# Kernel optimization log

Measured on AMD Instinct MI355X. Metric: run time of the kernel, lower is better.

## Reference

```python
import jax, jax.numpy as jnp
import numpy as np

B, T, F = 64, 96, 32          # batch, window_size, num_features
H_ENC, H_DEC = 128, 128       # encoder / decoder hidden sizes


def _lstm_cell(x, h, c, k, r, b):
    # Keras LSTMCell math: gates ordered i, f, g(candidate), o
    z = x @ k + h @ r + b
    i, f, g, o = jnp.split(z, 4, axis=-1)
    i = jax.nn.sigmoid(i)
    f = jax.nn.sigmoid(f)
    g = jnp.tanh(g)
    o = jax.nn.sigmoid(o)
    c_new = f * c + i * g
    h_new = o * jnp.tanh(c_new)
    return h_new, c_new


def setup_inputs() -> dict:
    key = jax.random.key(0)
    ks = jax.random.split(key, 20)
    s = 0.05
    d = {
        "inputs": jax.random.normal(ks[0], (B, T, F), jnp.float32),
        # encoder LSTMCell (input dim = F)
        "enc_k": jax.random.normal(ks[1], (F, 4 * H_ENC), jnp.float32) * s,
        "enc_r": jax.random.normal(ks[2], (H_ENC, 4 * H_ENC), jnp.float32) * s,
        "enc_b": jnp.zeros((4 * H_ENC,), jnp.float32),
        # encoder attention MLP: in = 2*H_ENC + T -> H_ENC -> 1
        "ae_w1": jax.random.normal(ks[3], (2 * H_ENC + T, H_ENC), jnp.float32) * s,
        "ae_b1": jnp.zeros((H_ENC,), jnp.float32),
        "ae_w2": jax.random.normal(ks[4], (H_ENC, 1), jnp.float32) * s,
        "ae_b2": jnp.zeros((1,), jnp.float32),
        # decoder LSTMCell (input dim = H_DEC, the fc output)
        "dec_k": jax.random.normal(ks[5], (H_DEC, 4 * H_DEC), jnp.float32) * s,
        "dec_r": jax.random.normal(ks[6], (H_DEC, 4 * H_DEC), jnp.float32) * s,
        "dec_b": jnp.zeros((4 * H_DEC,), jnp.float32),
        # decoder attention MLP: in = 2*H_DEC + H_ENC -> H_ENC -> 1
        "ad_w1": jax.random.normal(ks[7], (2 * H_DEC + H_ENC, H_ENC), jnp.float32) * s,
        "ad_b1": jnp.zeros((H_ENC,), jnp.float32),
        "ad_w2": jax.random.normal(ks[8], (H_ENC, 1), jnp.float32) * s,
        "ad_b2": jnp.zeros((1,), jnp.float32),
        # fc: (context H_ENC + y_prev 1) -> H_DEC
        "fc_w": jax.random.normal(ks[9], (H_ENC + 1, H_DEC), jnp.float32) * s,
        "fc_b": jnp.zeros((H_DEC,), jnp.float32),
        # fc_final: (d_n H_DEC + context H_ENC) -> F
        "ff_w": jax.random.normal(ks[10], (H_DEC + H_ENC, F), jnp.float32) * s,
        "ff_b": jnp.zeros((F,), jnp.float32),
    }
    return d


def reference(inputs, enc_k, enc_r, enc_b, ae_w1, ae_b1, ae_w2, ae_b2,
              dec_k, dec_r, dec_b, ad_w1, ad_b1, ad_w2, ad_b2,
              fc_w, fc_b, ff_w, ff_b):
    b, t, f = inputs.shape
    h_enc = enc_r.shape[0]
    h_dec = dec_r.shape[0]
    x_perm = jnp.transpose(inputs, (0, 2, 1))  # [B, F, T] (constant over time)

    # ---------------- encoder: input-attention LSTM over time ----------------
    def enc_step(carry, x_t):
        h, s = carry  # each [B, H_enc]
        hb = jnp.broadcast_to(h[:, None, :], (b, f, h_enc))
        sb = jnp.broadcast_to(s[:, None, :], (b, f, h_enc))
        cat = jnp.concatenate([hb, sb, x_perm], axis=2)       # [B, F, 2H+T]
        e = jnp.tanh(cat @ ae_w1 + ae_b1) @ ae_w2 + ae_b2     # [B, F, 1]
        alpha = jax.nn.softmax(e[..., 0], axis=1)             # [B, F]
        x_tilde = alpha * x_t                                 # [B, F]
        h, s = _lstm_cell(x_tilde, h, s, enc_k, enc_r, enc_b)
        return (h, s), h

    init = (jnp.zeros((b, h_enc), inputs.dtype), jnp.zeros((b, h_enc), inputs.dtype))
    _, h_all = jax.lax.scan(enc_step, init, jnp.transpose(inputs, (1, 0, 2)))
    x_encoded = jnp.transpose(h_all, (1, 0, 2))               # [B, T, H_enc]

    # ---------------- decoder: temporal-attention LSTM over time -------------
    y_prev = inputs[:, :, -1]                                 # [B, T]

    def dec_step(carry, y_t):
        d, c, _ = carry
        db = jnp.broadcast_to(d[:, None, :], (b, t, h_dec))
        cb = jnp.broadcast_to(c[:, None, :], (b, t, h_dec))
        cat = jnp.concatenate([db, cb, x_encoded], axis=2)    # [B, T, 2Hd+He]
        e = jnp.tanh(cat @ ad_w1 + ad_b1) @ ad_w2 + ad_b2     # [B, T, 1]
        beta = jax.nn.softmax(e[..., 0], axis=1)              # [B, T]
        ctx = jnp.einsum("bt,bth->bh", beta, x_encoded)       # [B, H_enc]
        y_tilde = jnp.concatenate([ctx, y_t[:, None]], axis=1) @ fc_w + fc_b
        d, c = _lstm_cell(y_tilde, d, c, dec_k, dec_r, dec_b)
        return (d, c, ctx), None

    init_d = (jnp.zeros((b, h_dec), inputs.dtype),
              jnp.zeros((b, h_dec), inputs.dtype),
              jnp.zeros((b, h_enc), inputs.dtype))
    (d_n, _, ctx), _ = jax.lax.scan(dec_step, init_d, jnp.transpose(y_prev, (1, 0)))

    y_pred = jnp.concatenate([d_n, ctx], axis=1) @ ff_w + ff_b  # [B, F]
    return y_pred[:, None, :]                                   # [B, 1, F]
```

## Files before the change

### kernel.cpp

```cpp
#include <hip/hip_runtime.h>

#define TT 96
#define FF 32
#define HH 128
#define G4 512
#define LOG2E 1.4426950408889634f

typedef _Float16 h2 __attribute__((ext_vector_type(2)));

__device__ __forceinline__ float fexp2(float x){ return __builtin_amdgcn_exp2f(x); }
__device__ __forceinline__ float frcp(float x){ return __builtin_amdgcn_rcpf(x); }
__device__ __forceinline__ float fsigmoid(float x){ return frcp(1.0f + fexp2(-LOG2E*x)); }
__device__ __forceinline__ float ftanh(float x){
    float u = fexp2(2.0f*LOG2E*x);
    return 1.0f - 2.0f*frcp(1.0f + u);
}
__device__ __forceinline__ h2 pk(float a, float b){
    h2 r; r.x = (_Float16)a; r.y = (_Float16)b; return r;
}
__device__ __forceinline__ unsigned pku(float a, float b){
    return __builtin_bit_cast(unsigned, pk(a, b));
}
__device__ __forceinline__ h2 u2h(unsigned v){ return __builtin_bit_cast(h2, v); }
__device__ __forceinline__ float fdot2(h2 a, h2 b, float c){
#if __has_builtin(__builtin_amdgcn_fdot2)
    return __builtin_amdgcn_fdot2(a, b, c, false);
#else
    return c + (float)a.x*(float)b.x + (float)a.y*(float)b.y;
#endif
}

__global__ __launch_bounds__(256) void k_prep(const float* __restrict__ fc_w,
                                              const float* __restrict__ fc_b,
                                              const float* __restrict__ dec_k,
                                              const float* __restrict__ dec_b,
                                              h2* __restrict__ Gp,
                                              float* __restrict__ gy,
                                              float* __restrict__ gb){
    int blk = blockIdx.x, tid = threadIdx.x;
    int u0 = tid, u1 = tid + 256;
    if (blk < 16){
        float a0[8], a1[8];
        #pragma unroll
        for (int r = 0; r < 8; ++r){ a0[r] = 0.f; a1[r] = 0.f; }
        for (int m = 0; m < 128; ++m){
            float d0 = dec_k[m*G4 + u0], d1 = dec_k[m*G4 + u1];
            #pragma unroll
            for (int r = 0; r < 8; ++r){
                float w = fc_w[(blk*8 + r)*HH + m];
                a0[r] += w * d0; a1[r] += w * d1;
            }
        }
        #pragma unroll
        for (int c = 0; c < 4; ++c){
            Gp[(blk*G4 + u0)*4 + c] = pk(a0[2*c], a0[2*c+1]);
            Gp[(blk*G4 + u1)*4 + c] = pk(a1[2*c], a1[2*c+1]);
        }
    } else if (blk == 16){
        float a0 = 0.f, a1 = 0.f;
        for (int m = 0; m < 128; ++m){
            float w = fc_w[128*HH + m];
            a0 += w * dec_k[m*G4 + u0]; a1 += w * dec_k[m*G4 + u1];
        }
        gy[u0] = a0; gy[u1] = a1;
    } else {
        float a0 = 0.f, a1 = 0.f;
        for (int m = 0; m < 128; ++m){
            float w = fc_b[m];
            a0 += w * dec_k[m*G4 + u0]; a1 += w * dec_k[m*G4 + u1];
        }
        gb[u0] = a0 + dec_b[u0]; gb[u1] = a1 + dec_b[u1];
    }
}

__global__ __launch_bounds__(1024)
__attribute__((amdgpu_waves_per_eu(4, 4)))
void k_enc(const float* __restrict__ inputs,
           const float* __restrict__ enc_k,
           const float* __restrict__ enc_r,
           const float* __restrict__ enc_b,
           const float* __restrict__ ae_w1,
           const float* __restrict__ ae_b1,
           const float* __restrict__ ae_w2,
           const float* __restrict__ ad_w1,
           float* __restrict__ ws_xenc,
           float* __restrict__ ws_xept){
    extern __shared__ float lds[];
    uint4* KLH4 = (uint4*)lds;
    float* XPJT = lds + 8192;
    float* XIN  = lds + 12416;
    float* HST  = lds + 15488;
    float* PP   = lds + 15744;
    float* PPZ  = lds + 16768;
    float* PE   = lds + 17792;
    float* W2E  = lds + 17920;
    float* AB1E = lds + 18048;
    h2*    HSP  = (h2*)(lds + 18176);
    h2*    XTP  = (h2*)(lds + 18240);
    uint4* WAE4 = (uint4*)(lds + 18256);
    _Float16* XEF = (_Float16*)(lds + 34640);

    const int b = blockIdx.x, tid = threadIdx.x;
    const int u = tid & 511, hf = tid >> 9;
    const int j7 = tid & 127, g8 = tid >> 7;
    const float* xin_g = inputs + b*TT*FF;

    for (int i = tid; i < TT*FF; i += 1024) XIN[i] = xin_g[i];
    for (int i = tid; i < 2048; i += 1024){
        int f8 = i >> 9, uu = i & 511;
        uint4 q;
        q.x = pku(enc_k[(f8*8+0)*G4+uu], enc_k[(f8*8+1)*G4+uu]);
        q.y = pku(enc_k[(f8*8+2)*G4+uu], enc_k[(f8*8+3)*G4+uu]);
        q.z = pku(enc_k[(f8*8+4)*G4+uu], enc_k[(f8*8+5)*G4+uu]);
        q.w = pku(enc_k[(f8*8+6)*G4+uu], enc_k[(f8*8+7)*G4+uu]);
        KLH4[i] = q;
    }
    for (int i = tid; i < 4096; i += 1024){
        int j = i & 127, i4g = i >> 7;
        int kbase = (i4g >> 2)*32 + (i4g & 3)*8;
        uint4 wv;
        wv.x = pku(ae_w1[(kbase+0)*HH + j], ae_w1[(kbase+1)*HH + j]);
        wv.y = pku(ae_w1[(kbase+2)*HH + j], ae_w1[(kbase+3)*HH + j]);
        wv.z = pku(ae_w1[(kbase+4)*HH + j], ae_w1[(kbase+5)*HH + j]);
        wv.w = pku(ae_w1[(kbase+6)*HH + j], ae_w1[(kbase+7)*HH + j]);
        WAE4[i] = wv;
    }
    if (tid < 128){ W2E[tid] = ae_w2[tid]; AB1E[tid] = ae_b1[tid]; HSP[tid] = pk(0.f, 0.f); }
    if (tid < 256) HST[tid] = 0.f;

    h2 rp_e[32];
    #pragma unroll
    for (int i = 0; i < 32; ++i)
        rp_e[i] = pk(enc_r[(hf*64 + 2*i)*G4 + u], enc_r[(hf*64 + 2*i+1)*G4 + u]);
    const float eb = (hf == 0) ? enc_b[u] : 0.f;
    __syncthreads();

    {
        int j = tid & 127, fh = tid >> 7;
        float a0=0.f, a1=0.f, a2=0.f, a3=0.f;
        for (int t = 0; t < TT; ++t){
            float w = ae_w1[(256 + t)*HH + j];
            const float* xr = &XIN[t*FF + fh*4];
            a0 += xr[0]*w; a1 += xr[1]*w; a2 += xr[2]*w; a3 += xr[3]*w;
        }
        XPJT[j*33 + fh*4 + 0] = a0;
        XPJT[j*33 + fh*4 + 1] = a1;
        XPJT[j*33 + fh*4 + 2] = a2;
        XPJT[j*33 + fh*4 + 3] = a3;
    }
    __syncthreads();

    const uint4* HSP4 = (const uint4*)HSP;
    const uint4* XTP4 = (const uint4*)XTP;

    for (int t = 0; t < TT; ++t){
        {
            float a0 = 0.f, a1 = 0.f;
            #pragma unroll
            for (int i4 = 0; i4 < 4; ++i4){
                uint4 q  = HSP4[g8*4 + i4];
                uint4 wv = WAE4[(g8*4 + i4)*128 + j7];
                a0 = fdot2(u2h(q.x), u2h(wv.x), a0);
                a1 = fdot2(u2h(q.y), u2h(wv.y), a1);
                a0 = fdot2(u2h(q.z), u2h(wv.z), a0);
                a1 = fdot2(u2h(q.w), u2h(wv.w), a1);
            }
            PP[tid] = a0 + a1;
        }
        float z = eb;
        {
            float z2 = 0.f;
            #pragma unroll
            for (int i4 = 0; i4 < 8; ++i4){
                uint4 q = HSP4[hf*8 + i4];
                z  = fdot2(u2h(q.x), rp_e[i4*4+0], z);
                z2 = fdot2(u2h(q.y), rp_e[i4*4+1], z2);
                z  = fdot2(u2h(q.z), rp_e[i4*4+2], z);
                z2 = fdot2(u2h(q.w), rp_e[i4*4+3], z2);
            }
            z += z2;
        }
        __syncthreads();
        if (tid < 128){
            float s = AB1E[tid];
            #pragma unroll
            for (int g = 0; g < 8; ++g) s += PP[tid + 128*g];
            PE[tid] = s;
        }
        __syncthreads();
        {
            int f = tid & 31, jg = tid >> 5;
            float acc = 0.f;
            #pragma unroll
            for (int i = 0; i < 4; ++i){
                int j = jg*4 + i;
                acc += ftanh(PE[j] + XPJT[j*33 + f]) * W2E[j];
            }
            PP[tid] = acc;
        }
        __syncthreads();
        if (tid < 32){
            float e = 0.f;
            #pragma unroll
            for (int g = 0; g < 32; ++g) e += PP[g*32 + tid];
            float p = fexp2(e * LOG2E);
            float ss = p;
            #pragma unroll
            for (int d = 16; d; d >>= 1) ss += __shfl_xor(ss, d, 32);
            float xt = p * frcp(ss) * XIN[t*FF + tid];
            float xt2 = __shfl_xor(xt, 1);
            if (!(tid & 1)) XTP[tid >> 1] = pk(xt, xt2);
        }
        __syncthreads();
        {
            float z2 = 0.f;
            #pragma unroll
            for (int c = 0; c < 2; ++c){
                int f8 = hf*2 + c;
                uint4 kq = KLH4[f8*512 + u];
                uint4 xq = XTP4[f8];
                z  = fdot2(u2h(kq.x), u2h(xq.x), z);
                z2 = fdot2(u2h(kq.y), u2h(xq.y), z2);
                z  = fdot2(u2h(kq.z), u2h(xq.z), z);
                z2 = fdot2(u2h(kq.w), u2h(xq.w), z2);
            }
            PPZ[hf*512 + u] = z + z2;
        }
        __syncthreads();
        if (tid < 128){
            int j = tid;
            float zi = PPZ[j]       + PPZ[512 + j];
            float zf = PPZ[128 + j] + PPZ[640 + j];
            float zg = PPZ[256 + j] + PPZ[768 + j];
            float zo = PPZ[384 + j] + PPZ[896 + j];
            float iv = fsigmoid(zi);
            float fv = fsigmoid(zf);
            float gv = ftanh(zg);
            float ov = fsigmoid(zo);
            float cn = fv * HST[128 + j] + iv * gv;
            float hn = ov * ftanh(cn);
            HST[128 + j] = cn;
            HST[j] = hn;
            ws_xenc[(b*TT + t)*HH + j] = hn;
            XEF[t*HH + j] = (_Float16)hn;
            float hn2 = __shfl_xor(hn, 1);
            float cn2 = __shfl_xor(cn, 1);
            if (!(j & 1)){
                HSP[j >> 1]        = pk(hn, hn2);
                HSP[64 + (j >> 1)] = pk(cn, cn2);
            }
        }
        __syncthreads();
    }

    {
        int j = tid & 127, th = tid >> 7;
        float acc[12];
        #pragma unroll
        for (int i = 0; i < 12; ++i) acc[i] = 0.f;
        for (int k = 0; k < 128; ++k){
            float w = ad_w1[(256 + k)*HH + j];
            #pragma unroll
            for (int i = 0; i < 12; ++i)
                acc[i] += (float)XEF[(th*12 + i)*HH + k] * w;
        }
        #pragma unroll
        for (int i = 0; i < 12; ++i)
            ws_xept[(b*HH + j)*TT + th*12 + i] = acc[i];
    }
}

__global__ __launch_bounds__(1024)
__attribute__((amdgpu_waves_per_eu(4, 4)))
void k_dec(const float* __restrict__ inputs,
           const float* __restrict__ dec_r,
           const float* __restrict__ ad_w1,
           const float* __restrict__ ad_b1,
           const float* __restrict__ ad_w2,
           const float* __restrict__ ff_w,
           const float* __restrict__ ff_b,
           const h2* __restrict__ Gp,
           const float* __restrict__ gy,
           const float* __restrict__ gb,
           const float* __restrict__ ws_xenc,
           const float* __restrict__ ws_xept,
           float* __restrict__ out){
    extern __shared__ float lds[];
    uint4* XE4 = (uint4*)lds;
    uint4* WDC4= (uint4*)(lds + 6144);
    float* PP  = lds + 22528;
    float* PPZ = lds + 23552;
    float* PPA = lds + 24576;
    float* APJ = lds + 25600;
    float* DST = lds + 25728;
    float* CTX = lds + 25984;
    float* W2L = lds + 26112;
    float* YV  = lds + 26240;
    float* SCAL= lds + 26336;
    h2*    DCP = (h2*)(lds + 26344);
    h2*    CXP = (h2*)(lds + 26408);
    h2*    BEP = (h2*)(lds + 26440);

    const int b = blockIdx.x, tid = threadIdx.x;
    const int u = tid & 511, hf = tid >> 9;
    const int j = tid & 127, og = tid >> 7;

    {
        const float* xe_g = ws_xenc + b*TT*HH;
        for (int i = tid; i < 12*HH; i += 1024){
            int t8 = i >> 7, k = i & 127;
            uint4 qq;
            qq.x = pku(xe_g[(t8*8 + 0)*HH + k], xe_g[(t8*8 + 1)*HH + k]);
            qq.y = pku(xe_g[(t8*8 + 2)*HH + k], xe_g[(t8*8 + 3)*HH + k]);
            qq.z = pku(xe_g[(t8*8 + 4)*HH + k], xe_g[(t8*8 + 5)*HH + k]);
            qq.w = pku(xe_g[(t8*8 + 6)*HH + k], xe_g[(t8*8 + 7)*HH + k]);
            XE4[i] = qq;
        }
    }
    for (int i = tid; i < 4096; i += 1024){
        int jj = i & 127, i4g = i >> 7;
        int kbase = (i4g >> 2)*32 + (i4g & 3)*8;
        uint4 wv;
        wv.x = pku(ad_w1[(kbase+0)*HH + jj], ad_w1[(kbase+1)*HH + jj]);
        wv.y = pku(ad_w1[(kbase+2)*HH + jj], ad_w1[(kbase+3)*HH + jj]);
        wv.z = pku(ad_w1[(kbase+4)*HH + jj], ad_w1[(kbase+5)*HH + jj]);
        wv.w = pku(ad_w1[(kbase+6)*HH + jj], ad_w1[(kbase+7)*HH + jj]);
        WDC4[i] = wv;
    }
    if (tid < TT) YV[tid] = inputs[b*TT*FF + tid*FF + (FF-1)];
    if (tid < 128){ W2L[tid] = ad_w2[tid]; DCP[tid] = pk(0.f, 0.f); }
    if (tid < 256) DST[tid] = 0.f;

    h2 rp[32];
    #pragma unroll
    for (int i = 0; i < 32; ++i)
        rp[i] = pk(dec_r[(hf*64 + 2*i)*G4 + u], dec_r[(hf*64 + 2*i+1)*G4 + u]);

    uint4 Greg[8];
    {
        const uint4* GQ = (const uint4*)Gp;
        #pragma unroll
        for (int g = 0; g < 8; ++g) Greg[g] = GQ[(hf*8 + g)*G4 + u];
    }

    float xpr[16];
    {
        const float* xp_g = ws_xept + (b*HH + og*16)*TT + j;
        if (j < TT){
            #pragma unroll
            for (int i = 0; i < 16; ++i) xpr[i] = xp_g[i*TT];
        } else {
            #pragma unroll
            for (int i = 0; i < 16; ++i) xpr[i] = 0.f;
        }
    }

    const float gbr = gb[u], gyr = gy[u];
    const float ab1 = (tid < 128) ? ad_b1[tid] : 0.f;
    __syncthreads();

    const uint4* DCP4 = (const uint4*)DCP;
    const uint4* CXP4 = (const uint4*)CXP;
    const uint4* BEP4 = (const uint4*)BEP;

    for (int t = 0; t < TT; ++t){
        float z = (hf == 0) ? (gbr + YV[t]*gyr) : 0.f;
        {
            float z2 = 0.f;
            #pragma unroll
            for (int i4 = 0; i4 < 8; ++i4){
                uint4 q = DCP4[hf*8 + i4];
                z  = fdot2(u2h(q.x), rp[i4*4+0], z);
                z2 = fdot2(u2h(q.y), rp[i4*4+1], z2);
                z  = fdot2(u2h(q.z), rp[i4*4+2], z);
                z2 = fdot2(u2h(q.w), rp[i4*4+3], z2);
            }
            z += z2;
        }
        {
            float s0 = 0.f, s1 = 0.f;
            #pragma unroll
            for (int i = 0; i < 4; ++i){
                uint4 dq = DCP4[og*4 + i];
                uint4 wv = WDC4[(og*4 + i)*128 + j];
                s0 = fdot2(u2h(dq.x), u2h(wv.x), s0);
                s1 = fdot2(u2h(dq.y), u2h(wv.y), s1);
                s0 = fdot2(u2h(dq.z), u2h(wv.z), s0);
                s1 = fdot2(u2h(dq.w), u2h(wv.w), s1);
            }
            PPA[og*128 + j] = s0 + s1;
        }
        __syncthreads();
        if (tid < 128){
            float s = ab1;
            #pragma unroll
            for (int g = 0; g < 8; ++g) s += PPA[tid + 128*g];
            APJ[tid] = s;
        }
        __syncthreads();
        {
            float acc = 0.f;
            if (j < TT){
                #pragma unroll
                for (int q4 = 0; q4 < 4; ++q4){
                    float4 aj = *(const float4*)&APJ[og*16 + q4*4];
                    float4 wj = *(const float4*)&W2L[og*16 + q4*4];
                    acc += ftanh(aj.x + xpr[q4*4+0]) * wj.x;
                    acc += ftanh(aj.y + xpr[q4*4+1]) * wj.y;
                    acc += ftanh(aj.z + xpr[q4*4+2]) * wj.z;
                    acc += ftanh(aj.w + xpr[q4*4+3]) * wj.w;
                }
            }
            PP[tid] = acc;
        }
        __syncthreads();
        if (tid < 64){
            float ea = 0.f;
            #pragma unroll
            for (int g = 0; g < 8; ++g) ea += PP[tid + 128*g];
            float pa = fexp2(ea * LOG2E);
            float pb = 0.f;
            if (tid < 32){
                float ebv = 0.f;
                #pragma unroll
                for (int g = 0; g < 8; ++g) ebv += PP[64 + tid + 128*g];
                pb = fexp2(ebv * LOG2E);
            }
            float ss = pa + pb;
            #pragma unroll
            for (int d = 32; d; d >>= 1) ss += __shfl_xor(ss, d, 64);
            float pa2 = __shfl_xor(pa, 1);
            float pb2 = __shfl_xor(pb, 1);
            if (!(tid & 1)){
                BEP[tid >> 1] = pk(pa, pa2);
                if (tid < 32) BEP[32 + (tid >> 1)] = pk(pb, pb2);
            }
            if (tid == 0) SCAL[0] = frcp(ss);
        }
        __syncthreads();
        if (tid < 128){
            float s0 = 0.f, s1 = 0.f;
            #pragma unroll
            for (int t8 = 0; t8 < 12; t8 += 2){
                uint4 xq0 = XE4[t8*HH + tid],     bb0 = BEP4[t8];
                uint4 xq1 = XE4[(t8+1)*HH + tid], bb1 = BEP4[t8+1];
                s0 = fdot2(u2h(xq0.x), u2h(bb0.x), s0);
                s1 = fdot2(u2h(xq0.y), u2h(bb0.y), s1);
                s0 = fdot2(u2h(xq0.z), u2h(bb0.z), s0);
                s1 = fdot2(u2h(xq0.w), u2h(bb0.w), s1);
                s0 = fdot2(u2h(xq1.x), u2h(bb1.x), s0);
                s1 = fdot2(u2h(xq1.y), u2h(bb1.y), s1);
                s0 = fdot2(u2h(xq1.z), u2h(bb1.z), s0);
                s1 = fdot2(u2h(xq1.w), u2h(bb1.w), s1);
            }
            float cv = (s0 + s1) * SCAL[0];
            CTX[tid] = cv;
            float cv2 = __shfl_xor(cv, 1);
            if (!(tid & 1)) CXP[tid >> 1] = pk(cv, cv2);
        }
        __syncthreads();
        {
            float z2 = 0.f;
            #pragma unroll
            for (int gi = 0; gi < 8; ++gi){
                uint4 q  = Greg[gi];
                uint4 cc = CXP4[hf*8 + gi];
                z  = fdot2(u2h(q.x), u2h(cc.x), z);
                z2 = fdot2(u2h(q.y), u2h(cc.y), z2);
                z  = fdot2(u2h(q.z), u2h(cc.z), z);
                z2 = fdot2(u2h(q.w), u2h(cc.w), z2);
            }
            PPZ[hf*512 + u] = z + z2;
        }
        __syncthreads();
        if (tid < 128){
            int jj = tid;
            float zi = PPZ[jj]       + PPZ[512 + jj];
            float zf = PPZ[128 + jj] + PPZ[640 + jj];
            float zg = PPZ[256 + jj] + PPZ[768 + jj];
            float zo = PPZ[384 + jj] + PPZ[896 + jj];
            float iv = fsigmoid(zi);
            float fv = fsigmoid(zf);
            float gv = ftanh(zg);
            float ov = fsigmoid(zo);
            float cn = fv * DST[128 + jj] + iv * gv;
            float hn = ov * ftanh(cn);
            DST[128 + jj] = cn;
            DST[jj] = hn;
            float hn2 = __shfl_xor(hn, 1);
            float cn2 = __shfl_xor(cn, 1);
            if (!(jj & 1)){
                DCP[jj >> 1]        = pk(hn, hn2);
                DCP[64 + (jj >> 1)] = pk(cn, cn2);
            }
        }
        __syncthreads();
    }

    {
        int jp = tid & 31, sg = tid >> 5;
        float a = 0.f;
        #pragma unroll
        for (int kk = 0; kk < 8; ++kk){
            int k = sg*8 + kk;
            float val = (k < 128) ? DST[k] : CTX[k - 128];
            a += val * ff_w[k*FF + jp];
        }
        PP[sg*32 + jp] = a;
    }
    __syncthreads();
    if (tid < 32){
        float o = ff_b[tid];
        #pragma unroll
        for (int s = 0; s < 32; ++s) o += PP[s*32 + tid];
        out[b*FF + tid] = o;
    }
}

extern "C" void kernel_launch(void* const* d_in, const int* in_sizes, int n_in,
                              void* d_out, int out_size, void* d_ws, size_t ws_size,
                              hipStream_t stream) {
    const float* inputs = (const float*)d_in[0];
    const float* enc_k  = (const float*)d_in[1];
    const float* enc_r  = (const float*)d_in[2];
    const float* enc_b  = (const float*)d_in[3];
    const float* ae_w1  = (const float*)d_in[4];
    const float* ae_b1  = (const float*)d_in[5];
    const float* ae_w2  = (const float*)d_in[6];
    const float* dec_k  = (const float*)d_in[8];
    const float* dec_r  = (const float*)d_in[9];
    const float* dec_b  = (const float*)d_in[10];
    const float* ad_w1  = (const float*)d_in[11];
    const float* ad_b1  = (const float*)d_in[12];
    const float* ad_w2  = (const float*)d_in[13];
    const float* fc_w   = (const float*)d_in[15];
    const float* fc_b   = (const float*)d_in[16];
    const float* ff_w   = (const float*)d_in[17];
    const float* ff_b   = (const float*)d_in[18];

    float* ws      = (float*)d_ws;
    float* ws_xenc = ws;
    float* ws_xept = ws + 786432;
    h2*    Gp      = (h2*)(ws + 1572864);
    float* gy      = ws + 1605632;
    float* gb      = ws + 1606144;

    hipFuncSetAttribute((const void*)k_enc, hipFuncAttributeMaxDynamicSharedMemorySize, 163136);
    hipFuncSetAttribute((const void*)k_dec, hipFuncAttributeMaxDynamicSharedMemorySize, 105888);

    k_prep<<<18, 256, 0, stream>>>(fc_w, fc_b, dec_k, dec_b, Gp, gy, gb);
    k_enc<<<64, 1024, 163136, stream>>>(inputs, enc_k, enc_r, enc_b, ae_w1, ae_b1, ae_w2,
                                        ad_w1, ws_xenc, ws_xept);
    k_dec<<<64, 1024, 105888, stream>>>(inputs, dec_r, ad_w1, ad_b1, ad_w2, ff_w, ff_b,
                                        Gp, gy, gb, ws_xenc, ws_xept, (float*)d_out);
}
```

Baseline: 810.1 us.

## Remove per-step barriers by computing attention projections on fewer threads

In both the encoder and decoder recurrences, the 1024-thread split-K dot product for the attention projection, which wrote partials to LDS and reduced them after a barrier, is replaced. Now 128 threads each compute the full 256-length dot product, which removes one __syncthreads per timestep and the partial-sum buffer. In the decoder, the softmax normalisation and the context reduction are merged into one 64-lane wave, dropping a second barrier and the SCAL slot. The waves_per_eu attribute is replaced with launch_bounds(1024,1). This trades more serial work per thread for fewer block-wide synchronisations on the latency-bound recurrent path.

```diff
diff --git a/kernel.cpp b/kernel.cpp
--- a/kernel.cpp
+++ b/kernel.cpp
@@ -73,8 +73,7 @@
     }
 }
 
-__global__ __launch_bounds__(1024)
-__attribute__((amdgpu_waves_per_eu(4, 4)))
+__global__ __launch_bounds__(1024, 1)
 void k_enc(const float* __restrict__ inputs,
            const float* __restrict__ enc_k,
            const float* __restrict__ enc_r,
@@ -102,7 +101,6 @@
 
     const int b = blockIdx.x, tid = threadIdx.x;
     const int u = tid & 511, hf = tid >> 9;
-    const int j7 = tid & 127, g8 = tid >> 7;
     const float* xin_g = inputs + b*TT*FF;
 
     for (int i = tid; i < TT*FF; i += 1024) XIN[i] = xin_g[i];
@@ -154,19 +152,6 @@
     const uint4* XTP4 = (const uint4*)XTP;
 
     for (int t = 0; t < TT; ++t){
-        {
-            float a0 = 0.f, a1 = 0.f;
-            #pragma unroll
-            for (int i4 = 0; i4 < 4; ++i4){
-                uint4 q  = HSP4[g8*4 + i4];
-                uint4 wv = WAE4[(g8*4 + i4)*128 + j7];
-                a0 = fdot2(u2h(q.x), u2h(wv.x), a0);
-                a1 = fdot2(u2h(q.y), u2h(wv.y), a1);
-                a0 = fdot2(u2h(q.z), u2h(wv.z), a0);
-                a1 = fdot2(u2h(q.w), u2h(wv.w), a1);
-            }
-            PP[tid] = a0 + a1;
-        }
         float z = eb;
         {
             float z2 = 0.f;
@@ -180,12 +165,22 @@
             }
             z += z2;
         }
-        __syncthreads();
         if (tid < 128){
-            float s = AB1E[tid];
-            #pragma unroll
-            for (int g = 0; g < 8; ++g) s += PP[tid + 128*g];
-            PE[tid] = s;
+            float s0 = 0.f, s1 = 0.f;
+            #pragma unroll
+            for (int m = 0; m < 32; m += 2){
+                uint4 dq0 = HSP4[m],     wv0 = WAE4[m*128 + tid];
+                uint4 dq1 = HSP4[m + 1], wv1 = WAE4[(m + 1)*128 + tid];
+                s0 = fdot2(u2h(dq0.x), u2h(wv0.x), s0);
+                s1 = fdot2(u2h(dq0.y), u2h(wv0.y), s1);
+                s0 = fdot2(u2h(dq0.z), u2h(wv0.z), s0);
+                s1 = fdot2(u2h(dq0.w), u2h(wv0.w), s1);
+                s0 = fdot2(u2h(dq1.x), u2h(wv1.x), s0);
+                s1 = fdot2(u2h(dq1.y), u2h(wv1.y), s1);
+                s0 = fdot2(u2h(dq1.z), u2h(wv1.z), s0);
+                s1 = fdot2(u2h(dq1.w), u2h(wv1.w), s1);
+            }
+            PE[tid] = s0 + s1 + AB1E[tid];
         }
         __syncthreads();
         {
@@ -270,8 +265,7 @@
     }
 }
 
-__global__ __launch_bounds__(1024)
-__attribute__((amdgpu_waves_per_eu(4, 4)))
+__global__ __launch_bounds__(1024, 1)
 void k_dec(const float* __restrict__ inputs,
            const float* __restrict__ dec_r,
            const float* __restrict__ ad_w1,
@@ -290,16 +284,14 @@
     uint4* WDC4= (uint4*)(lds + 6144);
     float* PP  = lds + 22528;
     float* PPZ = lds + 23552;
-    float* PPA = lds + 24576;
-    float* APJ = lds + 25600;
-    float* DST = lds + 25728;
-    float* CTX = lds + 25984;
-    float* W2L = lds + 26112;
-    float* YV  = lds + 26240;
-    float* SCAL= lds + 26336;
-    h2*    DCP = (h2*)(lds + 26344);
-    h2*    CXP = (h2*)(lds + 26408);
-    h2*    BEP = (h2*)(lds + 26440);
+    float* APJ = lds + 24576;
+    float* DST = lds + 24704;
+    float* CTX = lds + 24960;
+    float* W2L = lds + 25088;
+    float* YV  = lds + 25216;
+    h2*    DCP = (h2*)(lds + 25312);
+    h2*    CXP = (h2*)(lds + 25440);
+    h2*    BEP = (h2*)(lds + 25504);
 
     const int b = blockIdx.x, tid = threadIdx.x;
     const int u = tid & 511, hf = tid >> 9;
@@ -377,25 +369,22 @@
             }
             z += z2;
         }
-        {
+        if (tid < 128){
             float s0 = 0.f, s1 = 0.f;
             #pragma unroll
-            for (int i = 0; i < 4; ++i){
-                uint4 dq = DCP4[og*4 + i];
-                uint4 wv = WDC4[(og*4 + i)*128 + j];
-                s0 = fdot2(u2h(dq.x), u2h(wv.x), s0);
-                s1 = fdot2(u2h(dq.y), u2h(wv.y), s1);
-                s0 = fdot2(u2h(dq.z), u2h(wv.z), s0);
-                s1 = fdot2(u2h(dq.w), u2h(wv.w), s1);
-            }
-            PPA[og*128 + j] = s0 + s1;
-        }
-        __syncthreads();
-        if (tid < 128){
-            float s = ab1;
-            #pragma unroll
-            for (int g = 0; g < 8; ++g) s += PPA[tid + 128*g];
-            APJ[tid] = s;
+            for (int m = 0; m < 32; m += 2){
+                uint4 dq0 = DCP4[m],     wv0 = WDC4[m*128 + tid];
+                uint4 dq1 = DCP4[m + 1], wv1 = WDC4[(m + 1)*128 + tid];
+                s0 = fdot2(u2h(dq0.x), u2h(wv0.x), s0);
+                s1 = fdot2(u2h(dq0.y), u2h(wv0.y), s1);
+                s0 = fdot2(u2h(dq0.z), u2h(wv0.z), s0);
+                s1 = fdot2(u2h(dq0.w), u2h(wv0.w), s1);
+                s0 = fdot2(u2h(dq1.x), u2h(wv1.x), s0);
+                s1 = fdot2(u2h(dq1.y), u2h(wv1.y), s1);
+                s0 = fdot2(u2h(dq1.z), u2h(wv1.z), s0);
+                s1 = fdot2(u2h(dq1.w), u2h(wv1.w), s1);
+            }
+            APJ[tid] = s0 + s1 + ab1;
         }
         __syncthreads();
         {
@@ -415,48 +404,51 @@
         }
         __syncthreads();
         if (tid < 64){
+            int l = tid;
             float ea = 0.f;
             #pragma unroll
-            for (int g = 0; g < 8; ++g) ea += PP[tid + 128*g];
+            for (int g = 0; g < 8; ++g) ea += PP[l + 128*g];
             float pa = fexp2(ea * LOG2E);
             float pb = 0.f;
-            if (tid < 32){
+            if (l < 32){
                 float ebv = 0.f;
                 #pragma unroll
-                for (int g = 0; g < 8; ++g) ebv += PP[64 + tid + 128*g];
+                for (int g = 0; g < 8; ++g) ebv += PP[64 + l + 128*g];
                 pb = fexp2(ebv * LOG2E);
             }
             float ss = pa + pb;
             #pragma unroll
             for (int d = 32; d; d >>= 1) ss += __shfl_xor(ss, d, 64);
+            float rs = frcp(ss);
             float pa2 = __shfl_xor(pa, 1);
             float pb2 = __shfl_xor(pb, 1);
-            if (!(tid & 1)){
-                BEP[tid >> 1] = pk(pa, pa2);
-                if (tid < 32) BEP[32 + (tid >> 1)] = pk(pb, pb2);
-            }
-            if (tid == 0) SCAL[0] = frcp(ss);
-        }
-        __syncthreads();
-        if (tid < 128){
-            float s0 = 0.f, s1 = 0.f;
-            #pragma unroll
-            for (int t8 = 0; t8 < 12; t8 += 2){
-                uint4 xq0 = XE4[t8*HH + tid],     bb0 = BEP4[t8];
-                uint4 xq1 = XE4[(t8+1)*HH + tid], bb1 = BEP4[t8+1];
-                s0 = fdot2(u2h(xq0.x), u2h(bb0.x), s0);
-                s1 = fdot2(u2h(xq0.y), u2h(bb0.y), s1);
-                s0 = fdot2(u2h(xq0.z), u2h(bb0.z), s0);
-                s1 = fdot2(u2h(xq0.w), u2h(bb0.w), s1);
-                s0 = fdot2(u2h(xq1.x), u2h(bb1.x), s0);
-                s1 = fdot2(u2h(xq1.y), u2h(bb1.y), s1);
-                s0 = fdot2(u2h(xq1.z), u2h(bb1.z), s0);
-                s1 = fdot2(u2h(xq1.w), u2h(bb1.w), s1);
-            }
-            float cv = (s0 + s1) * SCAL[0];
-            CTX[tid] = cv;
-            float cv2 = __shfl_xor(cv, 1);
-            if (!(tid & 1)) CXP[tid >> 1] = pk(cv, cv2);
+            if (!(l & 1)){
+                BEP[l >> 1] = pk(pa, pa2);
+                if (l < 32) BEP[32 + (l >> 1)] = pk(pb, pb2);
+            }
+            float cva = 0.f, cvb = 0.f;
+            #pragma unroll
+            for (int t8 = 0; t8 < 12; ++t8){
+                uint4 bb = BEP4[t8];
+                uint4 xa = XE4[t8*HH + l];
+                uint4 xb = XE4[t8*HH + 64 + l];
+                cva = fdot2(u2h(xa.x), u2h(bb.x), cva);
+                cvb = fdot2(u2h(xb.x), u2h(bb.x), cvb);
+                cva = fdot2(u2h(xa.y), u2h(bb.y), cva);
+                cvb = fdot2(u2h(xb.y), u2h(bb.y), cvb);
+                cva = fdot2(u2h(xa.z), u2h(bb.z), cva);
+                cvb = fdot2(u2h(xb.z), u2h(bb.z), cvb);
+                cva = fdot2(u2h(xa.w), u2h(bb.w), cva);
+                cvb = fdot2(u2h(xb.w), u2h(bb.w), cvb);
+            }
+            cva *= rs; cvb *= rs;
+            CTX[l] = cva; CTX[64 + l] = cvb;
+            float cva2 = __shfl_xor(cva, 1);
+            float cvb2 = __shfl_xor(cvb, 1);
+            if (!(l & 1)){
+                CXP[l >> 1]        = pk(cva, cva2);
+                CXP[32 + (l >> 1)] = pk(cvb, cvb2);
+            }
         }
         __syncthreads();
         {
@@ -546,11 +538,11 @@
     float* gb      = ws + 1606144;
 
     hipFuncSetAttribute((const void*)k_enc, hipFuncAttributeMaxDynamicSharedMemorySize, 163136);
-    hipFuncSetAttribute((const void*)k_dec, hipFuncAttributeMaxDynamicSharedMemorySize, 105888);
+    hipFuncSetAttribute((const void*)k_dec, hipFuncAttributeMaxDynamicSharedMemorySize, 102272);
 
     k_prep<<<18, 256, 0, stream>>>(fc_w, fc_b, dec_k, dec_b, Gp, gy, gb);
     k_enc<<<64, 1024, 163136, stream>>>(inputs, enc_k, enc_r, enc_b, ae_w1, ae_b1, ae_w2,
                                         ad_w1, ws_xenc, ws_xept);
-    k_dec<<<64, 1024, 105888, stream>>>(inputs, dec_r, ad_w1, ad_b1, ad_w2, ff_w, ff_b,
+    k_dec<<<64, 1024, 102272, stream>>>(inputs, dec_r, ad_w1, ad_b1, ad_w2, ff_w, ff_b,
                                         Gp, gy, gb, ws_xenc, ws_xept, (float*)d_out);
 }
```

Measured after the change: 870.4 us. 7.4% more time.

## Move per-thread weight and encoder-state slices from LDS into registers

Applied to the files above, without the earlier changes.

Both the encoder and decoder kernels now keep their per-thread slices of the attention weights, encoder input kernel, encoded-state tiles and cell state in registers instead of LDS, which shrinks dynamic shared memory a lot. The decoder context reduction is spread across all 1024 threads with a partial-sum pass plus a reduction, instead of running on 128 threads. This is meant to remove LDS reads and bank traffic from the sequential per-timestep loop. In exchange it raises register pressure, which is why waves_per_eu is replaced by a launch bound of one block, and it adds an extra barrier per decoder step.

```diff
diff --git a/kernel.cpp b/kernel.cpp
--- a/kernel.cpp
+++ b/kernel.cpp
@@ -73,8 +73,7 @@
     }
 }
 
-__global__ __launch_bounds__(1024)
-__attribute__((amdgpu_waves_per_eu(4, 4)))
+__global__ __launch_bounds__(1024, 1)
 void k_enc(const float* __restrict__ inputs,
            const float* __restrict__ enc_k,
            const float* __restrict__ enc_r,
@@ -86,19 +85,14 @@
            float* __restrict__ ws_xenc,
            float* __restrict__ ws_xept){
     extern __shared__ float lds[];
-    uint4* KLH4 = (uint4*)lds;
-    float* XPJT = lds + 8192;
-    float* XIN  = lds + 12416;
-    float* HST  = lds + 15488;
-    float* PP   = lds + 15744;
-    float* PPZ  = lds + 16768;
-    float* PE   = lds + 17792;
-    float* W2E  = lds + 17920;
-    float* AB1E = lds + 18048;
-    h2*    HSP  = (h2*)(lds + 18176);
-    h2*    XTP  = (h2*)(lds + 18240);
-    uint4* WAE4 = (uint4*)(lds + 18256);
-    _Float16* XEF = (_Float16*)(lds + 34640);
+    float* XPJT = lds;
+    float* XIN  = lds + 4224;
+    float* PP   = lds + 7296;
+    float* PPZ  = lds + 8320;
+    float* PE   = lds + 9344;
+    h2*    HSP  = (h2*)(lds + 9472);
+    h2*    XTP  = (h2*)(lds + 9536);
+    _Float16* XEF = (_Float16*)(lds + 9544);
 
     const int b = blockIdx.x, tid = threadIdx.x;
     const int u = tid & 511, hf = tid >> 9;
@@ -106,33 +100,41 @@
     const float* xin_g = inputs + b*TT*FF;
 
     for (int i = tid; i < TT*FF; i += 1024) XIN[i] = xin_g[i];
-    for (int i = tid; i < 2048; i += 1024){
-        int f8 = i >> 9, uu = i & 511;
-        uint4 q;
-        q.x = pku(enc_k[(f8*8+0)*G4+uu], enc_k[(f8*8+1)*G4+uu]);
-        q.y = pku(enc_k[(f8*8+2)*G4+uu], enc_k[(f8*8+3)*G4+uu]);
-        q.z = pku(enc_k[(f8*8+4)*G4+uu], enc_k[(f8*8+5)*G4+uu]);
-        q.w = pku(enc_k[(f8*8+6)*G4+uu], enc_k[(f8*8+7)*G4+uu]);
-        KLH4[i] = q;
-    }
-    for (int i = tid; i < 4096; i += 1024){
-        int j = i & 127, i4g = i >> 7;
-        int kbase = (i4g >> 2)*32 + (i4g & 3)*8;
-        uint4 wv;
-        wv.x = pku(ae_w1[(kbase+0)*HH + j], ae_w1[(kbase+1)*HH + j]);
-        wv.y = pku(ae_w1[(kbase+2)*HH + j], ae_w1[(kbase+3)*HH + j]);
-        wv.z = pku(ae_w1[(kbase+4)*HH + j], ae_w1[(kbase+5)*HH + j]);
-        wv.w = pku(ae_w1[(kbase+6)*HH + j], ae_w1[(kbase+7)*HH + j]);
-        WAE4[i] = wv;
-    }
-    if (tid < 128){ W2E[tid] = ae_w2[tid]; AB1E[tid] = ae_b1[tid]; HSP[tid] = pk(0.f, 0.f); }
-    if (tid < 256) HST[tid] = 0.f;
+    if (tid < 128) HSP[tid] = pk(0.f, 0.f);
 
     h2 rp_e[32];
     #pragma unroll
     for (int i = 0; i < 32; ++i)
         rp_e[i] = pk(enc_r[(hf*64 + 2*i)*G4 + u], enc_r[(hf*64 + 2*i+1)*G4 + u]);
+
+    uint4 wae[4];
+    #pragma unroll
+    for (int i4 = 0; i4 < 4; ++i4){
+        int r0 = (g8*4 + i4)*8;
+        wae[i4].x = pku(ae_w1[(r0+0)*HH + j7], ae_w1[(r0+1)*HH + j7]);
+        wae[i4].y = pku(ae_w1[(r0+2)*HH + j7], ae_w1[(r0+3)*HH + j7]);
+        wae[i4].z = pku(ae_w1[(r0+4)*HH + j7], ae_w1[(r0+5)*HH + j7]);
+        wae[i4].w = pku(ae_w1[(r0+6)*HH + j7], ae_w1[(r0+7)*HH + j7]);
+    }
+
+    uint4 kreg[2];
+    #pragma unroll
+    for (int c = 0; c < 2; ++c){
+        int f8 = hf*2 + c;
+        kreg[c].x = pku(enc_k[(f8*8+0)*G4 + u], enc_k[(f8*8+1)*G4 + u]);
+        kreg[c].y = pku(enc_k[(f8*8+2)*G4 + u], enc_k[(f8*8+3)*G4 + u]);
+        kreg[c].z = pku(enc_k[(f8*8+4)*G4 + u], enc_k[(f8*8+5)*G4 + u]);
+        kreg[c].w = pku(enc_k[(f8*8+6)*G4 + u], enc_k[(f8*8+7)*G4 + u]);
+    }
+
+    const int f5 = tid & 31, jg = tid >> 5;
+    float w2r[4];
+    #pragma unroll
+    for (int i = 0; i < 4; ++i) w2r[i] = ae_w2[jg*4 + i];
+
+    const float ab1e = (tid < 128) ? ae_b1[tid] : 0.f;
     const float eb = (hf == 0) ? enc_b[u] : 0.f;
+    float cenc = 0.f;
     __syncthreads();
 
     {
@@ -150,6 +152,10 @@
     }
     __syncthreads();
 
+    float xpjt_r[4];
+    #pragma unroll
+    for (int i = 0; i < 4; ++i) xpjt_r[i] = XPJT[(jg*4 + i)*33 + f5];
+
     const uint4* HSP4 = (const uint4*)HSP;
     const uint4* XTP4 = (const uint4*)XTP;
 
@@ -159,7 +165,7 @@
             #pragma unroll
             for (int i4 = 0; i4 < 4; ++i4){
                 uint4 q  = HSP4[g8*4 + i4];
-                uint4 wv = WAE4[(g8*4 + i4)*128 + j7];
+                uint4 wv = wae[i4];
                 a0 = fdot2(u2h(q.x), u2h(wv.x), a0);
                 a1 = fdot2(u2h(q.y), u2h(wv.y), a1);
                 a0 = fdot2(u2h(q.z), u2h(wv.z), a0);
@@ -182,20 +188,17 @@
         }
         __syncthreads();
         if (tid < 128){
-            float s = AB1E[tid];
+            float s = ab1e;
             #pragma unroll
             for (int g = 0; g < 8; ++g) s += PP[tid + 128*g];
             PE[tid] = s;
         }
         __syncthreads();
         {
-            int f = tid & 31, jg = tid >> 5;
             float acc = 0.f;
             #pragma unroll
-            for (int i = 0; i < 4; ++i){
-                int j = jg*4 + i;
-                acc += ftanh(PE[j] + XPJT[j*33 + f]) * W2E[j];
-            }
+            for (int i = 0; i < 4; ++i)
+                acc += ftanh(PE[jg*4 + i] + xpjt_r[i]) * w2r[i];
             PP[tid] = acc;
         }
         __syncthreads();
@@ -216,9 +219,8 @@
             float z2 = 0.f;
             #pragma unroll
             for (int c = 0; c < 2; ++c){
-                int f8 = hf*2 + c;
-                uint4 kq = KLH4[f8*512 + u];
-                uint4 xq = XTP4[f8];
+                uint4 kq = kreg[c];
+                uint4 xq = XTP4[hf*2 + c];
                 z  = fdot2(u2h(kq.x), u2h(xq.x), z);
                 z2 = fdot2(u2h(kq.y), u2h(xq.y), z2);
                 z  = fdot2(u2h(kq.z), u2h(xq.z), z);
@@ -237,10 +239,9 @@
             float fv = fsigmoid(zf);
             float gv = ftanh(zg);
             float ov = fsigmoid(zo);
-            float cn = fv * HST[128 + j] + iv * gv;
+            float cn = fv * cenc + iv * gv;
             float hn = ov * ftanh(cn);
-            HST[128 + j] = cn;
-            HST[j] = hn;
+            cenc = cn;
             ws_xenc[(b*TT + t)*HH + j] = hn;
             XEF[t*HH + j] = (_Float16)hn;
             float hn2 = __shfl_xor(hn, 1);
@@ -270,8 +271,7 @@
     }
 }
 
-__global__ __launch_bounds__(1024)
-__attribute__((amdgpu_waves_per_eu(4, 4)))
+__global__ __launch_bounds__(1024, 1)
 void k_dec(const float* __restrict__ inputs,
            const float* __restrict__ dec_r,
            const float* __restrict__ ad_w1,
@@ -286,50 +286,25 @@
            const float* __restrict__ ws_xept,
            float* __restrict__ out){
     extern __shared__ float lds[];
-    uint4* XE4 = (uint4*)lds;
-    uint4* WDC4= (uint4*)(lds + 6144);
-    float* PP  = lds + 22528;
-    float* PPZ = lds + 23552;
-    float* PPA = lds + 24576;
-    float* APJ = lds + 25600;
-    float* DST = lds + 25728;
-    float* CTX = lds + 25984;
-    float* W2L = lds + 26112;
-    float* YV  = lds + 26240;
-    float* SCAL= lds + 26336;
-    h2*    DCP = (h2*)(lds + 26344);
-    h2*    CXP = (h2*)(lds + 26408);
-    h2*    BEP = (h2*)(lds + 26440);
+    float* PP  = lds;
+    float* PPZ = lds + 1024;
+    float* PPA = lds + 2048;
+    float* APJ = lds + 3072;
+    float* DST = lds + 3200;
+    float* CTX = lds + 3328;
+    float* W2L = lds + 3456;
+    float* YV  = lds + 3584;
+    float* SCAL= lds + 3680;
+    h2*    DCP = (h2*)(lds + 3688);
+    h2*    CXP = (h2*)(lds + 3752);
+    h2*    BEP = (h2*)(lds + 3784);
 
     const int b = blockIdx.x, tid = threadIdx.x;
     const int u = tid & 511, hf = tid >> 9;
     const int j = tid & 127, og = tid >> 7;
 
-    {
-        const float* xe_g = ws_xenc + b*TT*HH;
-        for (int i = tid; i < 12*HH; i += 1024){
-            int t8 = i >> 7, k = i & 127;
-            uint4 qq;
-            qq.x = pku(xe_g[(t8*8 + 0)*HH + k], xe_g[(t8*8 + 1)*HH + k]);
-            qq.y = pku(xe_g[(t8*8 + 2)*HH + k], xe_g[(t8*8 + 3)*HH + k]);
-            qq.z = pku(xe_g[(t8*8 + 4)*HH + k], xe_g[(t8*8 + 5)*HH + k]);
-            qq.w = pku(xe_g[(t8*8 + 6)*HH + k], xe_g[(t8*8 + 7)*HH + k]);
-            XE4[i] = qq;
-        }
-    }
-    for (int i = tid; i < 4096; i += 1024){
-        int jj = i & 127, i4g = i >> 7;
-        int kbase = (i4g >> 2)*32 + (i4g & 3)*8;
-        uint4 wv;
-        wv.x = pku(ad_w1[(kbase+0)*HH + jj], ad_w1[(kbase+1)*HH + jj]);
-        wv.y = pku(ad_w1[(kbase+2)*HH + jj], ad_w1[(kbase+3)*HH + jj]);
-        wv.z = pku(ad_w1[(kbase+4)*HH + jj], ad_w1[(kbase+5)*HH + jj]);
-        wv.w = pku(ad_w1[(kbase+6)*HH + jj], ad_w1[(kbase+7)*HH + jj]);
-        WDC4[i] = wv;
-    }
     if (tid < TT) YV[tid] = inputs[b*TT*FF + tid*FF + (FF-1)];
     if (tid < 128){ W2L[tid] = ad_w2[tid]; DCP[tid] = pk(0.f, 0.f); }
-    if (tid < 256) DST[tid] = 0.f;
 
     h2 rp[32];
     #pragma unroll
@@ -355,13 +330,38 @@
         }
     }
 
+    uint4 wreg[4];
+    #pragma unroll
+    for (int i = 0; i < 4; ++i){
+        int r0 = (og*4 + i)*8;
+        wreg[i].x = pku(ad_w1[(r0+0)*HH + j], ad_w1[(r0+1)*HH + j]);
+        wreg[i].y = pku(ad_w1[(r0+2)*HH + j], ad_w1[(r0+3)*HH + j]);
+        wreg[i].z = pku(ad_w1[(r0+4)*HH + j], ad_w1[(r0+5)*HH + j]);
+        wreg[i].w = pku(ad_w1[(r0+6)*HH + j], ad_w1[(r0+7)*HH + j]);
+    }
+
+    uint2 xe2[3];
+    {
+        const float* xe_g = ws_xenc + b*TT*HH + j;
+        #pragma unroll
+        for (int ii = 0; ii < 3; ++ii){
+            int h = og*3 + ii;
+            int t0 = h*4;
+            uint2 v;
+            v.x = pku(xe_g[(t0+0)*HH], xe_g[(t0+1)*HH]);
+            v.y = pku(xe_g[(t0+2)*HH], xe_g[(t0+3)*HH]);
+            xe2[ii] = v;
+        }
+    }
+
     const float gbr = gb[u], gyr = gy[u];
     const float ab1 = (tid < 128) ? ad_b1[tid] : 0.f;
+    float creg = 0.f;
     __syncthreads();
 
     const uint4* DCP4 = (const uint4*)DCP;
     const uint4* CXP4 = (const uint4*)CXP;
-    const uint4* BEP4 = (const uint4*)BEP;
+    const uint2* BEP2 = (const uint2*)BEP;
 
     for (int t = 0; t < TT; ++t){
         float z = (hf == 0) ? (gbr + YV[t]*gyr) : 0.f;
@@ -382,7 +382,7 @@
             #pragma unroll
             for (int i = 0; i < 4; ++i){
                 uint4 dq = DCP4[og*4 + i];
-                uint4 wv = WDC4[(og*4 + i)*128 + j];
+                uint4 wv = wreg[i];
                 s0 = fdot2(u2h(dq.x), u2h(wv.x), s0);
                 s1 = fdot2(u2h(dq.y), u2h(wv.y), s1);
                 s0 = fdot2(u2h(dq.z), u2h(wv.z), s0);
@@ -438,22 +438,22 @@
             if (tid == 0) SCAL[0] = frcp(ss);
         }
         __syncthreads();
+        {
+            float pc = 0.f;
+            #pragma unroll
+            for (int ii = 0; ii < 3; ++ii){
+                uint2 bb = BEP2[og*3 + ii];
+                pc = fdot2(u2h(xe2[ii].x), u2h(bb.x), pc);
+                pc = fdot2(u2h(xe2[ii].y), u2h(bb.y), pc);
+            }
+            PPA[og*128 + j] = pc;
+        }
+        __syncthreads();
         if (tid < 128){
-            float s0 = 0.f, s1 = 0.f;
-            #pragma unroll
-            for (int t8 = 0; t8 < 12; t8 += 2){
-                uint4 xq0 = XE4[t8*HH + tid],     bb0 = BEP4[t8];
-                uint4 xq1 = XE4[(t8+1)*HH + tid], bb1 = BEP4[t8+1];
-                s0 = fdot2(u2h(xq0.x), u2h(bb0.x), s0);
-                s1 = fdot2(u2h(xq0.y), u2h(bb0.y), s1);
-                s0 = fdot2(u2h(xq0.z), u2h(bb0.z), s0);
-                s1 = fdot2(u2h(xq0.w), u2h(bb0.w), s1);
-                s0 = fdot2(u2h(xq1.x), u2h(bb1.x), s0);
-                s1 = fdot2(u2h(xq1.y), u2h(bb1.y), s1);
-                s0 = fdot2(u2h(xq1.z), u2h(bb1.z), s0);
-                s1 = fdot2(u2h(xq1.w), u2h(bb1.w), s1);
-            }
-            float cv = (s0 + s1) * SCAL[0];
+            float cv = 0.f;
+            #pragma unroll
+            for (int g = 0; g < 8; ++g) cv += PPA[tid + 128*g];
+            cv *= SCAL[0];
             CTX[tid] = cv;
             float cv2 = __shfl_xor(cv, 1);
             if (!(tid & 1)) CXP[tid >> 1] = pk(cv, cv2);
@@ -483,9 +483,9 @@
             float fv = fsigmoid(zf);
             float gv = ftanh(zg);
             float ov = fsigmoid(zo);
-            float cn = fv * DST[128 + jj] + iv * gv;
+            float cn = fv * creg + iv * gv;
             float hn = ov * ftanh(cn);
-            DST[128 + jj] = cn;
+            creg = cn;
             DST[jj] = hn;
             float hn2 = __shfl_xor(hn, 1);
             float cn2 = __shfl_xor(cn, 1);
@@ -545,12 +545,12 @@
     float* gy      = ws + 1605632;
     float* gb      = ws + 1606144;
 
-    hipFuncSetAttribute((const void*)k_enc, hipFuncAttributeMaxDynamicSharedMemorySize, 163136);
-    hipFuncSetAttribute((const void*)k_dec, hipFuncAttributeMaxDynamicSharedMemorySize, 105888);
+    hipFuncSetAttribute((const void*)k_enc, hipFuncAttributeMaxDynamicSharedMemorySize, 62752);
+    hipFuncSetAttribute((const void*)k_dec, hipFuncAttributeMaxDynamicSharedMemorySize, 15264);
 
     k_prep<<<18, 256, 0, stream>>>(fc_w, fc_b, dec_k, dec_b, Gp, gy, gb);
-    k_enc<<<64, 1024, 163136, stream>>>(inputs, enc_k, enc_r, enc_b, ae_w1, ae_b1, ae_w2,
-                                        ad_w1, ws_xenc, ws_xept);
-    k_dec<<<64, 1024, 105888, stream>>>(inputs, dec_r, ad_w1, ad_b1, ad_w2, ff_w, ff_b,
-                                        Gp, gy, gb, ws_xenc, ws_xept, (float*)d_out);
-}
+    k_enc<<<64, 1024, 62752, stream>>>(inputs, enc_k, enc_r, enc_b, ae_w1, ae_b1, ae_w2,
+                                       ad_w1, ws_xenc, ws_xept);
+    k_dec<<<64, 1024, 15264, stream>>>(inputs, dec_r, ad_w1, ad_b1, ad_w2, ff_w, ff_b,
+                                       Gp, gy, gb, ws_xenc, ws_xept, (float*)d_out);
+}
```

New measurement: 904.2 us. 11.6% more time.
